# Optimization experiments

Measured on AMD Instinct MI355X. Metric: run time of the kernel, lower is better.

The kernel has to match this reference:

```python
import jax, jax.numpy as jnp
import numpy as np

B = 1024          # batch
INPUT_LEN = 4096  # dense width of incoming activation
OUT = 4096        # out_features
FAN_IN = 128      # in_features (fixed fan-in per output)


def setup_inputs() -> dict:
    key = jax.random.key(0)
    k1, k2, k3, k4 = jax.random.split(key, 4)
    bound = 1.0 / np.sqrt(FAN_IN)
    inp = jax.random.normal(k1, (B, INPUT_LEN), dtype=jnp.float32)
    weight = jax.random.uniform(k2, (OUT, FAN_IN), dtype=jnp.float32, minval=-bound, maxval=bound)
    bias = jax.random.uniform(k3, (OUT,), dtype=jnp.float32, minval=-bound, maxval=bound)
    indx_seqs = jax.random.randint(k4, (OUT, FAN_IN), 0, INPUT_LEN, dtype=jnp.int64 if jax.config.jax_enable_x64 else jnp.int32)
    return {"input": inp, "weight": weight, "bias": bias, "indx_seqs": indx_seqs}


def reference(input, weight, bias, indx_seqs):
    # gathered: (B, OUT, FAN_IN); weight broadcast over batch; reduce fan-in.
    gathered = input[:, indx_seqs]
    out = jnp.einsum('of,bof->bo', weight, gathered) + bias
    return out
```

## Files before the change

### kernel.cpp

```cpp
#include <hip/hip_runtime.h>
#include <stdint.h>

#define NB    1024
#define IL    4096
#define NOUT  4096
#define FI    128
#define BTILE 8
#define OSPLIT 4
#define OTILE (NOUT / OSPLIT)

__device__ __forceinline__ uint32_t rne_bf16_hi(float x) {
  uint32_t u = __float_as_uint(x);
  u += 0x7FFFu + ((u >> 16) & 1u);
  return u & 0xFFFF0000u;
}

__global__ __launch_bounds__(256)
void pack_kernel(const int* __restrict__ idx, const float* __restrict__ w,
                 uint32_t* __restrict__ pack) {
  int i = blockIdx.x * 256 + threadIdx.x;
  pack[i] = rne_bf16_hi(w[i]) | ((uint32_t)idx[i] & 0xFFFFu);
}

template<bool PACKED>
__global__ __launch_bounds__(1024)
void lincond_kernel(const float* __restrict__ input,
                    const uint32_t* __restrict__ pack,
                    const int*  __restrict__ idxs,
                    const float* __restrict__ wgt,
                    const float* __restrict__ bias,
                    float* __restrict__ out) {
  __shared__ uint32_t lds[IL * (BTILE / 2)];
  const int bid   = blockIdx.x;
  const int b0    = (bid >> 2) * BTILE;
  const int obase = (bid & 3) * OTILE;
  const int tid   = threadIdx.x;

  #pragma unroll
  for (int rep = 0; rep < 16; ++rep) {
    int e = rep * 1024 + tid;
    int d = e >> 12;
    int i = e & (IL - 1);
    float x0 = input[(size_t)(b0 + 2 * d)     * IL + i];
    float x1 = input[(size_t)(b0 + 2 * d + 1) * IL + i];
    lds[i * 4 + d] = rne_bf16_hi(x1) | (rne_bf16_hi(x0) >> 16);
  }
  __syncthreads();

  const int o = obase + tid;
  const uint4* rows = reinterpret_cast<const uint4*>(lds);
  float acc[8] = {0.f,0.f,0.f,0.f,0.f,0.f,0.f,0.f};

#define GBODY(IDXV, WV) {                                         \
    uint4 g = rows[(IDXV)];                                       \
    float wv = (WV);                                              \
    acc[0] = fmaf(wv, __uint_as_float(g.x << 16),         acc[0]);\
    acc[1] = fmaf(wv, __uint_as_float(g.x & 0xFFFF0000u), acc[1]);\
    acc[2] = fmaf(wv, __uint_as_float(g.y << 16),         acc[2]);\
    acc[3] = fmaf(wv, __uint_as_float(g.y & 0xFFFF0000u), acc[3]);\
    acc[4] = fmaf(wv, __uint_as_float(g.z << 16),         acc[4]);\
    acc[5] = fmaf(wv, __uint_as_float(g.z & 0xFFFF0000u), acc[5]);\
    acc[6] = fmaf(wv, __uint_as_float(g.w << 16),         acc[6]);\
    acc[7] = fmaf(wv, __uint_as_float(g.w & 0xFFFF0000u), acc[7]);}

#define PBODY(P) \
    GBODY((P.x & 0xFFFFu), __uint_as_float(P.x & 0xFFFF0000u)) \
    GBODY((P.y & 0xFFFFu), __uint_as_float(P.y & 0xFFFF0000u)) \
    GBODY((P.z & 0xFFFFu), __uint_as_float(P.z & 0xFFFF0000u)) \
    GBODY((P.w & 0xFFFFu), __uint_as_float(P.w & 0xFFFF0000u))

#define RBODY(IV, WV) \
    GBODY(((uint32_t)IV.x), WV.x) \
    GBODY(((uint32_t)IV.y), WV.y) \
    GBODY(((uint32_t)IV.z), WV.z) \
    GBODY(((uint32_t)IV.w), WV.w)

  if (PACKED) {
    const uint4* pw = reinterpret_cast<const uint4*>(pack) + (size_t)o * (FI / 4);
    #pragma unroll 2
    for (int j = 0; j < 8; ++j) {
      uint4 p0 = pw[j * 4 + 0];
      uint4 p1 = pw[j * 4 + 1];
      uint4 p2 = pw[j * 4 + 2];
      uint4 p3 = pw[j * 4 + 3];
      PBODY(p0) PBODY(p1) PBODY(p2) PBODY(p3)
    }
  } else {
    const int4*   ip = reinterpret_cast<const int4*>(idxs)  + (size_t)o * (FI / 4);
    const float4* wp = reinterpret_cast<const float4*>(wgt) + (size_t)o * (FI / 4);
    #pragma unroll 2
    for (int j = 0; j < 8; ++j) {
      int4   i0 = ip[j * 4 + 0], i1 = ip[j * 4 + 1], i2 = ip[j * 4 + 2], i3 = ip[j * 4 + 3];
      float4 w0 = wp[j * 4 + 0], w1 = wp[j * 4 + 1], w2 = wp[j * 4 + 2], w3 = wp[j * 4 + 3];
      RBODY(i0, w0) RBODY(i1, w1) RBODY(i2, w2) RBODY(i3, w3)
    }
  }

  const float bv = bias[o];
  #pragma unroll
  for (int k = 0; k < 8; ++k) {
    out[(size_t)(b0 + k) * NOUT + o] = acc[k] + bv;
  }
}

extern "C" void kernel_launch(void* const* d_in, const int* in_sizes, int n_in,
                              void* d_out, int out_size, void* d_ws, size_t ws_size,
                              hipStream_t stream) {
  const float* input  = (const float*)d_in[0];
  const float* weight = (const float*)d_in[1];
  const float* bias   = (const float*)d_in[2];
  const int*   idxs   = (const int*)d_in[3];
  float*       out    = (float*)d_out;

  const size_t pack_bytes = (size_t)NOUT * FI * sizeof(uint32_t);
  const int grid = (NB / BTILE) * OSPLIT;

  if (ws_size >= pack_bytes) {
    uint32_t* pack = (uint32_t*)d_ws;
    pack_kernel<<<(NOUT * FI) / 256, 256, 0, stream>>>(idxs, weight, pack);
    lincond_kernel<true><<<grid, 1024, 0, stream>>>(input, pack, nullptr, nullptr, bias, out);
  } else {
    lincond_kernel<false><<<grid, 1024, 0, stream>>>(input, nullptr, idxs, weight, bias, out);
  }
}
```

Before: 55.66 us.

## Pre-pack bf16 input slabs and stream them into LDS via global_load_lds

Adds a separate slab kernel that converts and interleaves each 8-row batch tile of the input into bf16 pairs in workspace. The main kernel then fills LDS with direct global-to-LDS loads instead of per-block conversion and scattered LDS stores. The packed index is also pre-shifted to a byte offset, which saves a shift per gather. The extra kernel writes and rereads an 8 MB slab and needs a larger workspace, and if the workspace is too small the code falls back to the old path.

```diff
diff --git a/kernel.cpp b/kernel.cpp
--- a/kernel.cpp
+++ b/kernel.cpp
@@ -8,6 +8,7 @@
 #define BTILE 8
 #define OSPLIT 4
 #define OTILE (NOUT / OSPLIT)
+#define SLAB_DW (IL * (BTILE / 2))
 
 __device__ __forceinline__ uint32_t rne_bf16_hi(float x) {
   uint32_t u = __float_as_uint(x);
@@ -19,40 +20,67 @@
 void pack_kernel(const int* __restrict__ idx, const float* __restrict__ w,
                  uint32_t* __restrict__ pack) {
   int i = blockIdx.x * 256 + threadIdx.x;
-  pack[i] = rne_bf16_hi(w[i]) | ((uint32_t)idx[i] & 0xFFFFu);
+  pack[i] = rne_bf16_hi(w[i]) | (((uint32_t)idx[i] << 4) & 0xFFFFu);
 }
 
-template<bool PACKED>
+__global__ __launch_bounds__(256)
+void slab_kernel(const float* __restrict__ in, uint32_t* __restrict__ slab) {
+  int t = blockIdx.x * 256 + threadIdx.x;
+  int g = t >> 12;
+  int i = t & (IL - 1);
+  const float* base = in + (size_t)g * (8 * IL) + i;
+  uint4 v;
+  v.x = rne_bf16_hi(base[1 * IL]) | (rne_bf16_hi(base[0 * IL]) >> 16);
+  v.y = rne_bf16_hi(base[3 * IL]) | (rne_bf16_hi(base[2 * IL]) >> 16);
+  v.z = rne_bf16_hi(base[5 * IL]) | (rne_bf16_hi(base[4 * IL]) >> 16);
+  v.w = rne_bf16_hi(base[7 * IL]) | (rne_bf16_hi(base[6 * IL]) >> 16);
+  reinterpret_cast<uint4*>(slab)[t] = v;
+}
+
+template<int MODE>
 __global__ __launch_bounds__(1024)
 void lincond_kernel(const float* __restrict__ input,
+                    const uint32_t* __restrict__ slab,
                     const uint32_t* __restrict__ pack,
                     const int*  __restrict__ idxs,
                     const float* __restrict__ wgt,
                     const float* __restrict__ bias,
                     float* __restrict__ out) {
-  __shared__ uint32_t lds[IL * (BTILE / 2)];
+  __shared__ uint32_t lds[SLAB_DW];
   const int bid   = blockIdx.x;
   const int b0    = (bid >> 2) * BTILE;
   const int obase = (bid & 3) * OTILE;
   const int tid   = threadIdx.x;
 
-  #pragma unroll
-  for (int rep = 0; rep < 16; ++rep) {
-    int e = rep * 1024 + tid;
-    int d = e >> 12;
-    int i = e & (IL - 1);
-    float x0 = input[(size_t)(b0 + 2 * d)     * IL + i];
-    float x1 = input[(size_t)(b0 + 2 * d + 1) * IL + i];
-    lds[i * 4 + d] = rne_bf16_hi(x1) | (rne_bf16_hi(x0) >> 16);
+  if (MODE == 2) {
+    const uint32_t* src = slab + (size_t)(b0 >> 3) * SLAB_DW;
+    #pragma unroll
+    for (int r = 0; r < 4; ++r) {
+      int e = (r * 1024 + tid) * 4;
+      __builtin_amdgcn_global_load_lds(
+          (const __attribute__((address_space(1))) uint32_t*)(src + e),
+          (__attribute__((address_space(3))) uint32_t*)(lds + e),
+          16, 0, 0);
+    }
+  } else {
+    #pragma unroll
+    for (int rep = 0; rep < 16; ++rep) {
+      int e = rep * 1024 + tid;
+      int d = e >> 12;
+      int i = e & (IL - 1);
+      float x0 = input[(size_t)(b0 + 2 * d)     * IL + i];
+      float x1 = input[(size_t)(b0 + 2 * d + 1) * IL + i];
+      lds[i * 4 + d] = rne_bf16_hi(x1) | (rne_bf16_hi(x0) >> 16);
+    }
   }
   __syncthreads();
 
   const int o = obase + tid;
-  const uint4* rows = reinterpret_cast<const uint4*>(lds);
+  const char* ldsb = reinterpret_cast<const char*>(lds);
   float acc[8] = {0.f,0.f,0.f,0.f,0.f,0.f,0.f,0.f};
 
-#define GBODY(IDXV, WV) {                                         \
-    uint4 g = rows[(IDXV)];                                       \
+#define GBODY(OFF, WV) {                                          \
+    uint4 g = *reinterpret_cast<const uint4*>(ldsb + (OFF));      \
     float wv = (WV);                                              \
     acc[0] = fmaf(wv, __uint_as_float(g.x << 16),         acc[0]);\
     acc[1] = fmaf(wv, __uint_as_float(g.x & 0xFFFF0000u), acc[1]);\
@@ -70,12 +98,12 @@
     GBODY((P.w & 0xFFFFu), __uint_as_float(P.w & 0xFFFF0000u))
 
 #define RBODY(IV, WV) \
-    GBODY(((uint32_t)IV.x), WV.x) \
-    GBODY(((uint32_t)IV.y), WV.y) \
-    GBODY(((uint32_t)IV.z), WV.z) \
-    GBODY(((uint32_t)IV.w), WV.w)
+    GBODY(((uint32_t)IV.x << 4), WV.x) \
+    GBODY(((uint32_t)IV.y << 4), WV.y) \
+    GBODY(((uint32_t)IV.z << 4), WV.z) \
+    GBODY(((uint32_t)IV.w << 4), WV.w)
 
-  if (PACKED) {
+  if (MODE >= 1) {
     const uint4* pw = reinterpret_cast<const uint4*>(pack) + (size_t)o * (FI / 4);
     #pragma unroll 2
     for (int j = 0; j < 8; ++j) {
@@ -113,13 +141,20 @@
   float*       out    = (float*)d_out;
 
   const size_t pack_bytes = (size_t)NOUT * FI * sizeof(uint32_t);
+  const size_t slab_bytes = (size_t)(NB / BTILE) * SLAB_DW * sizeof(uint32_t);
   const int grid = (NB / BTILE) * OSPLIT;
 
-  if (ws_size >= pack_bytes) {
+  if (ws_size >= pack_bytes + slab_bytes) {
+    uint32_t* pack = (uint32_t*)d_ws;
+    uint32_t* slab = (uint32_t*)((char*)d_ws + pack_bytes);
+    pack_kernel<<<(NOUT * FI) / 256, 256, 0, stream>>>(idxs, weight, pack);
+    slab_kernel<<<(NB / BTILE) * IL / 256, 256, 0, stream>>>(input, slab);
+    lincond_kernel<2><<<grid, 1024, 0, stream>>>(input, slab, pack, nullptr, nullptr, bias, out);
+  } else if (ws_size >= pack_bytes) {
     uint32_t* pack = (uint32_t*)d_ws;
     pack_kernel<<<(NOUT * FI) / 256, 256, 0, stream>>>(idxs, weight, pack);
-    lincond_kernel<true><<<grid, 1024, 0, stream>>>(input, pack, nullptr, nullptr, bias, out);
+    lincond_kernel<1><<<grid, 1024, 0, stream>>>(input, nullptr, pack, nullptr, nullptr, bias, out);
   } else {
-    lincond_kernel<false><<<grid, 1024, 0, stream>>>(input, nullptr, idxs, weight, bias, out);
+    lincond_kernel<0><<<grid, 1024, 0, stream>>>(input, nullptr, nullptr, idxs, weight, bias, out);
   }
 }
```

After: 57.37 us. +3.1%, slower.
